# Optimization experiments

Measured on AMD Instinct MI355X. Metric: run time of the kernel, lower is better.

The kernel has to match this reference:

```python
import jax, jax.numpy as jnp
import numpy as np

MEM = 2048

def _linear_params(key, scale):
    kw, kb = jax.random.split(key)
    W = jax.random.uniform(kw, (MEM, MEM), jnp.float32, -scale, scale)
    b = jax.random.uniform(kb, (MEM,), jnp.float32, -scale, scale)
    return W, b

def setup_inputs() -> dict:
    key = jax.random.key(0)
    ks = jax.random.split(key, 18)
    scale = 1.0 / np.sqrt(MEM)
    inp = {
        'lc': jax.random.normal(ks[0], (1, MEM), jnp.float32),
        'lh': jax.random.normal(ks[1], (1, MEM), jnp.float32),
        'rc': jax.random.normal(ks[2], (1, MEM), jnp.float32),
        'rh': jax.random.normal(ks[3], (1, MEM), jnp.float32),
        'S': jax.random.normal(ks[4], (1, MEM), jnp.float32),
        'w': jax.random.normal(ks[5], (1, MEM), jnp.float32),
    }
    names = ['Wh', 'Us', 'ma', 'ilh', 'irh', 'lflh', 'lfrh', 'rflh', 'rfrh', 'ulh', 'urh']
    for i, n in enumerate(names):
        W, b = _linear_params(ks[6 + i], scale)
        inp[n + '_w'] = W
        inp[n + '_b'] = b
    return inp

def _lin(x, W, b):
    return x @ W.T + b

def reference(lc, lh, rc, rh, S, w,
              Wh_w, Wh_b, Us_w, Us_b, ma_w, ma_b,
              ilh_w, ilh_b, irh_w, irh_b,
              lflh_w, lflh_b, lfrh_w, lfrh_b,
              rflh_w, rflh_b, rfrh_w, rfrh_b,
              ulh_w, ulh_b, urh_w, urh_b):
    # attention scoring over the two children
    m_left = jnp.tanh(_lin(lh, Wh_w, Wh_b) + _lin(S, Us_w, Us_b)).squeeze()   # [MEM]
    m_right = jnp.tanh(_lin(rh, Wh_w, Wh_b) + _lin(S, Us_w, Us_b)).squeeze()  # [MEM]
    exp_left = w @ m_left[:, None]    # [1,1]
    exp_right = w @ m_right[:, None]  # [1,1]
    denom = exp_left + exp_right
    left_alpha = exp_left / denom
    right_alpha = exp_right / denom
    # attention-weighted child hidden states
    la = jnp.tanh(_lin(left_alpha * lh, ma_w, ma_b))   # [1,MEM]
    ra = jnp.tanh(_lin(right_alpha * rh, ma_w, ma_b))  # [1,MEM]
    # tree-LSTM gates
    i = jax.nn.sigmoid(_lin(la, ilh_w, ilh_b) + _lin(ra, irh_w, irh_b))
    lf = jax.nn.sigmoid(_lin(la, lflh_w, lflh_b) + _lin(ra, lfrh_w, lfrh_b))
    rf = jax.nn.sigmoid(_lin(la, rflh_w, rflh_b) + _lin(ra, rfrh_w, rfrh_b))
    update = jnp.tanh(_lin(la, ulh_w, ulh_b) + _lin(ra, urh_w, urh_b))
    c = i * update + lf * lc + rf * rc
    h = jnp.tanh(c)
    return (c, h)
```

## Files before the change

### kernel.cpp

```cpp
#include <hip/hip_runtime.h>
#include <math.h>

#define MEM  2048
#define NT   256

struct Params {
    const float *lc, *rc, *lh, *rh, *S, *w;
    const float *Wh_w, *Wh_b, *Us_w, *Us_b, *ma_w, *ma_b;
    const float *ilh_w, *ilh_b, *irh_w, *irh_b;
    const float *lflh_w, *lflh_b, *lfrh_w, *lfrh_b;
    const float *rflh_w, *rflh_b, *rfrh_w, *rfrh_b;
    const float *ulh_w, *ulh_b, *urh_w, *urh_b;
    float *pl, *pr, *wml, *wmr, *out;
};

__device__ __forceinline__ float dot4(float4 a, float4 b) {
    return a.x * b.x + a.y * b.y + a.z * b.z + a.w * b.w;
}

__device__ __forceinline__ float wave_reduce(float v) {
#pragma unroll
    for (int off = 32; off > 0; off >>= 1)
        v += __shfl_down(v, off, 64);
    return v;
}

__device__ __forceinline__ float tanh_fast(float x) {
    x = fminf(15.0f, fmaxf(-15.0f, x));
    const float e = __expf(2.0f * x);
    return (e - 1.0f) / (e + 1.0f);
}
__device__ __forceinline__ float sigmoid_fast(float x) {
    return 1.0f / (1.0f + __expf(-x));
}

__global__ __launch_bounds__(NT) void k1(Params p)
{
    __shared__ float s_red[4][5];

    const int t   = threadIdx.x;
    const int row = blockIdx.x;

    const float4* wh4 = (const float4*)(p.Wh_w + (size_t)row * MEM);
    const float4* us4 = (const float4*)(p.Us_w + (size_t)row * MEM);
    const float4* ma4 = (const float4*)(p.ma_w + (size_t)row * MEM);
    const float4* l4  = (const float4*)p.lh;
    const float4* r4  = (const float4*)p.rh;
    const float4* s4  = (const float4*)p.S;

    float awl = 0.f, awr = 0.f, aus = 0.f, aml = 0.f, amr = 0.f;
#pragma unroll
    for (int h = 0; h < 2; ++h) {
        const int i = t + h * NT;
        const float4 a  = wh4[i];
        const float4 u  = us4[i];
        const float4 m  = ma4[i];
        const float4 xl = l4[i];
        const float4 xr = r4[i];
        const float4 xs = s4[i];
        awl += dot4(a, xl);
        awr += dot4(a, xr);
        aus += dot4(u, xs);
        aml += dot4(m, xl);
        amr += dot4(m, xr);
    }
    awl = wave_reduce(awl);
    awr = wave_reduce(awr);
    aus = wave_reduce(aus);
    aml = wave_reduce(aml);
    amr = wave_reduce(amr);

    const int wv = t >> 6, ln = t & 63;
    if (ln == 0) {
        s_red[wv][0] = awl; s_red[wv][1] = awr; s_red[wv][2] = aus;
        s_red[wv][3] = aml; s_red[wv][4] = amr;
    }
    __syncthreads();
    if (t == 0) {
        float r0 = 0.f, r1 = 0.f, r2 = 0.f, r3 = 0.f, r4v = 0.f;
#pragma unroll
        for (int k = 0; k < 4; ++k) {
            r0 += s_red[k][0]; r1 += s_red[k][1]; r2 += s_red[k][2];
            r3 += s_red[k][3]; r4v += s_red[k][4];
        }
        const float us = r2 + p.Us_b[row];
        const float ml = tanh_fast(r0 + p.Wh_b[row] + us);
        const float mr = tanh_fast(r1 + p.Wh_b[row] + us);
        p.pl[row] = r3;
        p.pr[row] = r4v;
        const float wj = p.w[row];
        p.wml[row] = wj * ml;
        p.wmr[row] = wj * mr;
    }
}

__global__ __launch_bounds__(NT, 8) void k2(Params p)
{
    __shared__ __align__(16) float s_xa[MEM];
    __shared__ __align__(16) float s_xb[MEM];
    __shared__ float s_red[4][2];
    __shared__ float s_g[4];
    __shared__ float s_al[2];

    const int t   = threadIdx.x;
    const int wv  = t >> 6, ln = t & 63;
    const int row = blockIdx.x;

    const float bI  = p.ilh_b[row]  + p.irh_b[row];
    const float bLF = p.lflh_b[row] + p.lfrh_b[row];
    const float bRF = p.rflh_b[row] + p.rfrh_b[row];
    const float bU  = p.ulh_b[row]  + p.urh_b[row];
    const float lcv = p.lc[row], rcv = p.rc[row];

    {
        const float4* wl4 = (const float4*)p.wml;
        const float4* wr4 = (const float4*)p.wmr;
        const float4 a0 = wl4[t], a1 = wl4[t + NT];
        const float4 b0 = wr4[t], b1 = wr4[t + NT];
        float el = a0.x + a0.y + a0.z + a0.w + a1.x + a1.y + a1.z + a1.w;
        float er = b0.x + b0.y + b0.z + b0.w + b1.x + b1.y + b1.z + b1.w;
        el = wave_reduce(el);
        er = wave_reduce(er);
        if (ln == 0) { s_red[wv][0] = el; s_red[wv][1] = er; }
    }
    __syncthreads();
    if (t == 0) {
        const float el = s_red[0][0] + s_red[1][0] + s_red[2][0] + s_red[3][0];
        const float er = s_red[0][1] + s_red[1][1] + s_red[2][1] + s_red[3][1];
        const float d  = el + er;
        s_al[0] = el / d;
        s_al[1] = er / d;
    }
    __syncthreads();
    const float al = s_al[0];
    const float ar = s_al[1];

    {
        const float4* p4 = (const float4*)p.pl;
        const float4* q4 = (const float4*)p.pr;
        const float4* b4 = (const float4*)p.ma_b;
        float4* sxa4 = (float4*)s_xa;
        float4* sxb4 = (float4*)s_xb;
#pragma unroll
        for (int h = 0; h < 2; ++h) {
            const int i = t + h * NT;
            const float4 pp = p4[i];
            const float4 qq = q4[i];
            const float4 bb = b4[i];
            float4 xa, xb;
            xa.x = tanh_fast(al * pp.x + bb.x); xb.x = tanh_fast(ar * qq.x + bb.x);
            xa.y = tanh_fast(al * pp.y + bb.y); xb.y = tanh_fast(ar * qq.y + bb.y);
            xa.z = tanh_fast(al * pp.z + bb.z); xb.z = tanh_fast(ar * qq.z + bb.z);
            xa.w = tanh_fast(al * pp.w + bb.w); xb.w = tanh_fast(ar * qq.w + bb.w);
            sxa4[i] = xa;
            sxb4[i] = xb;
        }
    }
    __syncthreads();

    const float *wlp, *wrp;
    if      (wv == 0) { wlp = p.ilh_w;  wrp = p.irh_w;  }
    else if (wv == 1) { wlp = p.lflh_w; wrp = p.lfrh_w; }
    else if (wv == 2) { wlp = p.rflh_w; wrp = p.rfrh_w; }
    else              { wlp = p.ulh_w;  wrp = p.urh_w;  }

    const float4* wl4 = (const float4*)(wlp + (size_t)row * MEM);
    const float4* wr4 = (const float4*)(wrp + (size_t)row * MEM);
    const float4* xa4 = (const float4*)s_xa;
    const float4* xb4 = (const float4*)s_xb;

    float accA = 0.f, accB = 0.f;
#pragma unroll
    for (int j = 0; j < 8; ++j) {
        const int i = ln + 64 * j;
        accA += dot4(wl4[i], xa4[i]);
        accB += dot4(wr4[i], xb4[i]);
    }
    const float g = wave_reduce(accA + accB);
    if (ln == 0) s_g[wv] = g;
    __syncthreads();

    if (t == 0) {
        const float ig  = sigmoid_fast(s_g[0] + bI);
        const float lfg = sigmoid_fast(s_g[1] + bLF);
        const float rfg = sigmoid_fast(s_g[2] + bRF);
        const float ug  = tanh_fast(s_g[3] + bU);
        const float c   = ig * ug + lfg * lcv + rfg * rcv;
        p.out[row]       = c;
        p.out[MEM + row] = tanh_fast(c);
    }
}

extern "C" void kernel_launch(void* const* d_in, const int* in_sizes, int n_in,
                              void* d_out, int out_size, void* d_ws, size_t ws_size,
                              hipStream_t stream)
{
    Params h;
    h.lc = (const float*)d_in[0];
    h.lh = (const float*)d_in[1];
    h.rc = (const float*)d_in[2];
    h.rh = (const float*)d_in[3];
    h.S  = (const float*)d_in[4];
    h.w  = (const float*)d_in[5];
    h.Wh_w   = (const float*)d_in[6];   h.Wh_b   = (const float*)d_in[7];
    h.Us_w   = (const float*)d_in[8];   h.Us_b   = (const float*)d_in[9];
    h.ma_w   = (const float*)d_in[10];  h.ma_b   = (const float*)d_in[11];
    h.ilh_w  = (const float*)d_in[12];  h.ilh_b  = (const float*)d_in[13];
    h.irh_w  = (const float*)d_in[14];  h.irh_b  = (const float*)d_in[15];
    h.lflh_w = (const float*)d_in[16];  h.lflh_b = (const float*)d_in[17];
    h.lfrh_w = (const float*)d_in[18];  h.lfrh_b = (const float*)d_in[19];
    h.rflh_w = (const float*)d_in[20];  h.rflh_b = (const float*)d_in[21];
    h.rfrh_w = (const float*)d_in[22];  h.rfrh_b = (const float*)d_in[23];
    h.ulh_w  = (const float*)d_in[24];  h.ulh_b  = (const float*)d_in[25];
    h.urh_w  = (const float*)d_in[26];  h.urh_b  = (const float*)d_in[27];

    float* ws = (float*)d_ws;
    h.pl  = ws;
    h.pr  = ws + MEM;
    h.wml = ws + 2 * MEM;
    h.wmr = ws + 3 * MEM;
    h.out = (float*)d_out;

    k1<<<MEM, NT, 0, stream>>>(h);
    k2<<<MEM, NT, 0, stream>>>(h);
}
```

Baseline: 241.3 us.

## Split alpha/activation stage into single-block kernel and prefetch weight rows into registers

The attention-alpha reduction and the tanh activations of la/ra move out of every k2 block into a separate one-block kernel that writes the activations to global workspace. Previously all 2048 k2 blocks recomputed them redundantly and staged 16KB of LDS each. k1 now gives each wave one weight matrix (Wh, Us, ma) with 192 threads. Both matrix-vector kernels issue all eight float4 weight loads up front into registers before the dot products. The cost is an extra serial kernel launch, and the activation vectors are now read from global/L2 instead of LDS.

```diff
diff --git a/kernel.cpp b/kernel.cpp
--- a/kernel.cpp
+++ b/kernel.cpp
@@ -3,6 +3,7 @@
 
 #define MEM  2048
 #define NT   256
+#define NT1  192
 
 struct Params {
     const float *lc, *rc, *lh, *rh, *S, *w;
@@ -34,73 +35,126 @@
     return 1.0f / (1.0f + __expf(-x));
 }
 
-__global__ __launch_bounds__(NT) void k1(Params p)
-{
-    __shared__ float s_red[4][5];
+__global__ __launch_bounds__(NT1, 2) void k1(Params p)
+{
+    __shared__ float s_par[5];
 
     const int t   = threadIdx.x;
+    const int wv  = t >> 6, ln = t & 63;
     const int row = blockIdx.x;
 
-    const float4* wh4 = (const float4*)(p.Wh_w + (size_t)row * MEM);
-    const float4* us4 = (const float4*)(p.Us_w + (size_t)row * MEM);
-    const float4* ma4 = (const float4*)(p.ma_w + (size_t)row * MEM);
-    const float4* l4  = (const float4*)p.lh;
-    const float4* r4  = (const float4*)p.rh;
-    const float4* s4  = (const float4*)p.S;
-
-    float awl = 0.f, awr = 0.f, aus = 0.f, aml = 0.f, amr = 0.f;
-#pragma unroll
-    for (int h = 0; h < 2; ++h) {
-        const int i = t + h * NT;
-        const float4 a  = wh4[i];
-        const float4 u  = us4[i];
-        const float4 m  = ma4[i];
-        const float4 xl = l4[i];
-        const float4 xr = r4[i];
-        const float4 xs = s4[i];
-        awl += dot4(a, xl);
-        awr += dot4(a, xr);
-        aus += dot4(u, xs);
-        aml += dot4(m, xl);
-        amr += dot4(m, xr);
-    }
-    awl = wave_reduce(awl);
-    awr = wave_reduce(awr);
-    aus = wave_reduce(aus);
-    aml = wave_reduce(aml);
-    amr = wave_reduce(amr);
-
-    const int wv = t >> 6, ln = t & 63;
-    if (ln == 0) {
-        s_red[wv][0] = awl; s_red[wv][1] = awr; s_red[wv][2] = aus;
-        s_red[wv][3] = aml; s_red[wv][4] = amr;
-    }
-    __syncthreads();
+    const float4* l4 = (const float4*)p.lh;
+    const float4* r4 = (const float4*)p.rh;
+    const float4* s4 = (const float4*)p.S;
+
+    if (wv == 0) {
+        const float4* w4 = (const float4*)(p.Wh_w + (size_t)row * MEM);
+        float4 wb[8];
+#pragma unroll
+        for (int j = 0; j < 8; ++j) wb[j] = w4[ln + 64 * j];
+        float awl = 0.f, awr = 0.f;
+#pragma unroll
+        for (int j = 0; j < 8; ++j) {
+            awl += dot4(wb[j], l4[ln + 64 * j]);
+            awr += dot4(wb[j], r4[ln + 64 * j]);
+        }
+        awl = wave_reduce(awl);
+        awr = wave_reduce(awr);
+        if (ln == 0) { s_par[0] = awl; s_par[1] = awr; }
+    } else if (wv == 1) {
+        const float4* u4 = (const float4*)(p.Us_w + (size_t)row * MEM);
+        float4 ub[8];
+#pragma unroll
+        for (int j = 0; j < 8; ++j) ub[j] = u4[ln + 64 * j];
+        float aus = 0.f;
+#pragma unroll
+        for (int j = 0; j < 8; ++j)
+            aus += dot4(ub[j], s4[ln + 64 * j]);
+        aus = wave_reduce(aus);
+        if (ln == 0) s_par[2] = aus;
+    } else {
+        const float4* m4 = (const float4*)(p.ma_w + (size_t)row * MEM);
+        float4 mb[8];
+#pragma unroll
+        for (int j = 0; j < 8; ++j) mb[j] = m4[ln + 64 * j];
+        float aml = 0.f, amr = 0.f;
+#pragma unroll
+        for (int j = 0; j < 8; ++j) {
+            aml += dot4(mb[j], l4[ln + 64 * j]);
+            amr += dot4(mb[j], r4[ln + 64 * j]);
+        }
+        aml = wave_reduce(aml);
+        amr = wave_reduce(amr);
+        if (ln == 0) { s_par[3] = aml; s_par[4] = amr; }
+    }
+    __syncthreads();
+
     if (t == 0) {
-        float r0 = 0.f, r1 = 0.f, r2 = 0.f, r3 = 0.f, r4v = 0.f;
-#pragma unroll
-        for (int k = 0; k < 4; ++k) {
-            r0 += s_red[k][0]; r1 += s_red[k][1]; r2 += s_red[k][2];
-            r3 += s_red[k][3]; r4v += s_red[k][4];
-        }
-        const float us = r2 + p.Us_b[row];
-        const float ml = tanh_fast(r0 + p.Wh_b[row] + us);
-        const float mr = tanh_fast(r1 + p.Wh_b[row] + us);
-        p.pl[row] = r3;
-        p.pr[row] = r4v;
+        const float us  = s_par[2] + p.Us_b[row];
+        const float whb = p.Wh_b[row];
+        const float ml  = tanh_fast(s_par[0] + whb + us);
+        const float mr  = tanh_fast(s_par[1] + whb + us);
+        p.pl[row] = s_par[3];
+        p.pr[row] = s_par[4];
         const float wj = p.w[row];
         p.wml[row] = wj * ml;
         p.wmr[row] = wj * mr;
     }
 }
 
-__global__ __launch_bounds__(NT, 8) void k2(Params p)
-{
-    __shared__ __align__(16) float s_xa[MEM];
-    __shared__ __align__(16) float s_xb[MEM];
+__global__ __launch_bounds__(NT) void kmid(Params p)
+{
     __shared__ float s_red[4][2];
+    __shared__ float s_al[2];
+
+    const int t  = threadIdx.x;
+    const int wv = t >> 6, ln = t & 63;
+
+    const float4* wl4 = (const float4*)p.wml;
+    const float4* wr4 = (const float4*)p.wmr;
+    const float4 a0 = wl4[t], a1 = wl4[t + NT];
+    const float4 b0 = wr4[t], b1 = wr4[t + NT];
+    float el = a0.x + a0.y + a0.z + a0.w + a1.x + a1.y + a1.z + a1.w;
+    float er = b0.x + b0.y + b0.z + b0.w + b1.x + b1.y + b1.z + b1.w;
+    el = wave_reduce(el);
+    er = wave_reduce(er);
+    if (ln == 0) { s_red[wv][0] = el; s_red[wv][1] = er; }
+    __syncthreads();
+    if (t == 0) {
+        const float e0 = s_red[0][0] + s_red[1][0] + s_red[2][0] + s_red[3][0];
+        const float e1 = s_red[0][1] + s_red[1][1] + s_red[2][1] + s_red[3][1];
+        const float d  = e0 + e1;
+        s_al[0] = e0 / d;
+        s_al[1] = e1 / d;
+    }
+    __syncthreads();
+    const float al = s_al[0];
+    const float ar = s_al[1];
+
+    const float4* p4 = (const float4*)p.pl;
+    const float4* q4 = (const float4*)p.pr;
+    const float4* b4 = (const float4*)p.ma_b;
+    float4* xa4 = (float4*)p.wml;
+    float4* xb4 = (float4*)p.wmr;
+#pragma unroll
+    for (int h = 0; h < 2; ++h) {
+        const int i = t + h * NT;
+        const float4 pp = p4[i];
+        const float4 qq = q4[i];
+        const float4 bb = b4[i];
+        float4 xa, xb;
+        xa.x = tanh_fast(al * pp.x + bb.x); xb.x = tanh_fast(ar * qq.x + bb.x);
+        xa.y = tanh_fast(al * pp.y + bb.y); xb.y = tanh_fast(ar * qq.y + bb.y);
+        xa.z = tanh_fast(al * pp.z + bb.z); xb.z = tanh_fast(ar * qq.z + bb.z);
+        xa.w = tanh_fast(al * pp.w + bb.w); xb.w = tanh_fast(ar * qq.w + bb.w);
+        xa4[i] = xa;
+        xb4[i] = xb;
+    }
+}
+
+__global__ __launch_bounds__(NT, 2) void k2(Params p)
+{
     __shared__ float s_g[4];
-    __shared__ float s_al[2];
 
     const int t   = threadIdx.x;
     const int wv  = t >> 6, ln = t & 63;
@@ -112,70 +166,29 @@
     const float bU  = p.ulh_b[row]  + p.urh_b[row];
     const float lcv = p.lc[row], rcv = p.rc[row];
 
-    {
-        const float4* wl4 = (const float4*)p.wml;
-        const float4* wr4 = (const float4*)p.wmr;
-        const float4 a0 = wl4[t], a1 = wl4[t + NT];
-        const float4 b0 = wr4[t], b1 = wr4[t + NT];
-        float el = a0.x + a0.y + a0.z + a0.w + a1.x + a1.y + a1.z + a1.w;
-        float er = b0.x + b0.y + b0.z + b0.w + b1.x + b1.y + b1.z + b1.w;
-        el = wave_reduce(el);
-        er = wave_reduce(er);
-        if (ln == 0) { s_red[wv][0] = el; s_red[wv][1] = er; }
-    }
-    __syncthreads();
-    if (t == 0) {
-        const float el = s_red[0][0] + s_red[1][0] + s_red[2][0] + s_red[3][0];
-        const float er = s_red[0][1] + s_red[1][1] + s_red[2][1] + s_red[3][1];
-        const float d  = el + er;
-        s_al[0] = el / d;
-        s_al[1] = er / d;
-    }
-    __syncthreads();
-    const float al = s_al[0];
-    const float ar = s_al[1];
-
-    {
-        const float4* p4 = (const float4*)p.pl;
-        const float4* q4 = (const float4*)p.pr;
-        const float4* b4 = (const float4*)p.ma_b;
-        float4* sxa4 = (float4*)s_xa;
-        float4* sxb4 = (float4*)s_xb;
-#pragma unroll
-        for (int h = 0; h < 2; ++h) {
-            const int i = t + h * NT;
-            const float4 pp = p4[i];
-            const float4 qq = q4[i];
-            const float4 bb = b4[i];
-            float4 xa, xb;
-            xa.x = tanh_fast(al * pp.x + bb.x); xb.x = tanh_fast(ar * qq.x + bb.x);
-            xa.y = tanh_fast(al * pp.y + bb.y); xb.y = tanh_fast(ar * qq.y + bb.y);
-            xa.z = tanh_fast(al * pp.z + bb.z); xb.z = tanh_fast(ar * qq.z + bb.z);
-            xa.w = tanh_fast(al * pp.w + bb.w); xb.w = tanh_fast(ar * qq.w + bb.w);
-            sxa4[i] = xa;
-            sxb4[i] = xb;
-        }
-    }
-    __syncthreads();
-
     const float *wlp, *wrp;
     if      (wv == 0) { wlp = p.ilh_w;  wrp = p.irh_w;  }
     else if (wv == 1) { wlp = p.lflh_w; wrp = p.lfrh_w; }
     else if (wv == 2) { wlp = p.rflh_w; wrp = p.rfrh_w; }
     else              { wlp = p.ulh_w;  wrp = p.urh_w;  }
 
-    const float4* wl4 = (const float4*)(wlp + (size_t)row * MEM);
-    const float4* wr4 = (const float4*)(wrp + (size_t)row * MEM);
-    const float4* xa4 = (const float4*)s_xa;
-    const float4* xb4 = (const float4*)s_xb;
+    const float4* wl4  = (const float4*)(wlp + (size_t)row * MEM);
+    const float4* wr4  = (const float4*)(wrp + (size_t)row * MEM);
+    const float4* xag4 = (const float4*)p.wml;
+    const float4* xbg4 = (const float4*)p.wmr;
+
+    float4 ab[8], bb[8];
+#pragma unroll
+    for (int j = 0; j < 8; ++j) ab[j] = wl4[ln + 64 * j];
+#pragma unroll
+    for (int j = 0; j < 8; ++j) bb[j] = wr4[ln + 64 * j];
 
     float accA = 0.f, accB = 0.f;
 #pragma unroll
-    for (int j = 0; j < 8; ++j) {
-        const int i = ln + 64 * j;
-        accA += dot4(wl4[i], xa4[i]);
-        accB += dot4(wr4[i], xb4[i]);
-    }
+    for (int j = 0; j < 8; ++j) accA += dot4(ab[j], xag4[ln + 64 * j]);
+#pragma unroll
+    for (int j = 0; j < 8; ++j) accB += dot4(bb[j], xbg4[ln + 64 * j]);
+
     const float g = wave_reduce(accA + accB);
     if (ln == 0) s_g[wv] = g;
     __syncthreads();
@@ -221,6 +234,7 @@
     h.wmr = ws + 3 * MEM;
     h.out = (float*)d_out;
 
-    k1<<<MEM, NT, 0, stream>>>(h);
-    k2<<<MEM, NT, 0, stream>>>(h);
-}
+    k1  <<<MEM, NT1, 0, stream>>>(h);
+    kmid<<<1,   NT,  0, stream>>>(h);
+    k2  <<<MEM, NT,  0, stream>>>(h);
+}
```

Result: no change. 242.8 us (+0.6%).
